# Optimization experiments

Measured on AMD Instinct MI355X. Metric: run time of the kernel, lower is better.

Reference implementation:

```python
import jax, jax.numpy as jnp
import numpy as np

B, S, E, H = 2, 2048, 1024, 16
DH = E // H  # 64
FF = 4 * E


def setup_inputs() -> dict:
    key = jax.random.key(0)
    ks = jax.random.split(key, 13)
    s = 0.02
    return {
        "x": jax.random.normal(ks[0], (B, S, E), dtype=jnp.float32),
        "Wq": jax.random.normal(ks[1], (H, E, DH), dtype=jnp.float32) * s,
        "Wk": jax.random.normal(ks[2], (H, E, DH), dtype=jnp.float32) * s,
        "Wv": jax.random.normal(ks[3], (H, E, DH), dtype=jnp.float32) * s,
        "Wo": jax.random.normal(ks[4], (E, E), dtype=jnp.float32) * s,
        "bo": jnp.zeros((E,), dtype=jnp.float32),
        "W1": jax.random.normal(ks[5], (E, FF), dtype=jnp.float32) * s,
        "b1": jnp.zeros((FF,), dtype=jnp.float32),
        "W2": jax.random.normal(ks[6], (FF, E), dtype=jnp.float32) * s,
        "b2": jnp.zeros((E,), dtype=jnp.float32),
        "g1": jnp.ones((E,), dtype=jnp.float32),
        "beta1": jnp.zeros((E,), dtype=jnp.float32),
        "g2": jnp.ones((E,), dtype=jnp.float32),
        "beta2": jnp.zeros((E,), dtype=jnp.float32),
    }


def _layernorm(x, g, b, eps=1e-5):
    mu = jnp.mean(x, axis=-1, keepdims=True)
    var = jnp.var(x, axis=-1, keepdims=True)
    return (x - mu) * jax.lax.rsqrt(var + eps) * g + b


def reference(x, Wq, Wk, Wv, Wo, bo, W1, b1, W2, b2, g1, beta1, g2, beta2):
    # Pre-LN attention (dropout is identity in eval mode)
    nx = _layernorm(x, g1, beta1)
    # per-head projections, batched over heads: [B,H,S,DH]
    q = jnp.einsum('bse,hed->bhsd', nx, Wq)
    k = jnp.einsum('bse,hed->bhsd', nx, Wk)
    v = jnp.einsum('bse,hed->bhsd', nx, Wv)
    scores = jnp.einsum('bhqd,bhkd->bhqk', q, k) * (DH ** -0.5)  # [B,H,S,S]
    seq = x.shape[1]
    causal = jnp.tril(jnp.ones((seq, seq), dtype=bool))
    scores = jnp.where(causal, scores, -jnp.inf)
    w = jax.nn.softmax(scores, axis=-1)
    attn = jnp.einsum('bhqk,bhkd->bhqd', w, v)  # [B,H,S,DH]
    # concat heads (head order matches ModuleList cat order)
    attn = attn.transpose(0, 2, 1, 3).reshape(x.shape[0], seq, E)
    attn_out = attn @ Wo + bo
    x = x + attn_out
    # FFN
    nx2 = _layernorm(x, g2, beta2)
    ffn = jax.nn.relu(nx2 @ W1 + b1) @ W2 + b2
    return x + ffn
```

## Files before the change

kernel.cpp:

```cpp
#include <hip/hip_runtime.h>


typedef __attribute__((ext_vector_type(8))) short short8;
typedef __attribute__((ext_vector_type(4))) float floatx4;

__device__ inline unsigned short f32_to_bf16(float f) {
  unsigned u = __float_as_uint(f);
  unsigned rb = (u >> 16) & 1u;
  u += 0x7fffu + rb;
  return (unsigned short)(u >> 16);
}
__device__ inline unsigned f32_to_bf16_hi(float f) {
  return (__float_as_uint(f) + 0x8000u) >> 16;
}
__device__ inline float bf16_to_f32(unsigned short u) {
  return __uint_as_float(((unsigned)u) << 16);
}

__device__ inline void gload16(const void* g, void* l) {
  __builtin_amdgcn_global_load_lds(
      (const __attribute__((address_space(1))) void*)g,
      (__attribute__((address_space(3))) void*)l, 16, 0, 0);
}

__global__ __launch_bounds__(256) void transpose_to_bf16(
    const float* __restrict__ in, unsigned short* __restrict__ out,
    int R, int C, int ldo, long in_bs, long out_bs) {
  __shared__ float tile[32][33];
  in  += (size_t)blockIdx.z * in_bs;
  out += (size_t)blockIdx.z * out_bs;
  const int c0 = blockIdx.x * 32, r0 = blockIdx.y * 32;
  const int tx = threadIdx.x & 31, ty = threadIdx.x >> 5;
#pragma unroll
  for (int i = 0; i < 32; i += 8)
    tile[ty + i][tx] = in[(size_t)(r0 + ty + i) * C + c0 + tx];
  __syncthreads();
#pragma unroll
  for (int i = 0; i < 32; i += 8)
    out[(size_t)(c0 + ty + i) * ldo + r0 + tx] = f32_to_bf16(tile[tx][ty + i]);
}

__global__ __launch_bounds__(256) void transpose_qkv_to_bf16(
    const float* __restrict__ Wq, const float* __restrict__ Wk,
    const float* __restrict__ Wv, unsigned short* __restrict__ out) {
  __shared__ float tile[32][33];
  const int z = blockIdx.z, m = z >> 4;
  const float* in = (m == 0 ? Wq : (m == 1 ? Wk : Wv)) + (size_t)(z & 15) * 65536;
  unsigned short* o = out + (size_t)z * 65536;
  const int c0 = blockIdx.x * 32, r0 = blockIdx.y * 32;
  const int tx = threadIdx.x & 31, ty = threadIdx.x >> 5;
#pragma unroll
  for (int i = 0; i < 32; i += 8)
    tile[ty + i][tx] = in[(size_t)(r0 + ty + i) * 64 + c0 + tx];
  __syncthreads();
#pragma unroll
  for (int i = 0; i < 32; i += 8)
    o[(size_t)(c0 + ty + i) * 1024 + r0 + tx] = f32_to_bf16(tile[tx][ty + i]);
}

__global__ __launch_bounds__(256) void transpose_v(
    const unsigned short* __restrict__ qkv, unsigned short* __restrict__ vT) {
  __shared__ unsigned short tile[32][33];
  const int bh = blockIdx.z, b = bh >> 4, h = bh & 15;
  const int k0 = blockIdx.x * 32, d0 = blockIdx.y * 32;
  const int tx = threadIdx.x & 31, ty = threadIdx.x >> 5;
#pragma unroll
  for (int i = 0; i < 32; i += 8)
    tile[ty + i][tx] = qkv[(size_t)(b * 2048 + k0 + ty + i) * 3072 + 2048 + h * 64 + d0 + tx];
  __syncthreads();
#pragma unroll
  for (int i = 0; i < 32; i += 8)
    vT[((size_t)bh * 64 + d0 + ty + i) * 2048 + k0 + tx] = tile[tx][ty + i];
}

__global__ __launch_bounds__(256) void layernorm_bf16(
    const float* __restrict__ x, const float* __restrict__ g,
    const float* __restrict__ be, unsigned short* __restrict__ out) {
  const int row = blockIdx.x;
  const int t = threadIdx.x;
  floatx4 v = ((const floatx4*)(x + (size_t)row * 1024))[t];
  float s  = v[0] + v[1] + v[2] + v[3];
  float s2 = v[0]*v[0] + v[1]*v[1] + v[2]*v[2] + v[3]*v[3];
#pragma unroll
  for (int off = 1; off < 64; off <<= 1) {
    s  += __shfl_xor(s, off);
    s2 += __shfl_xor(s2, off);
  }
  __shared__ float red[8];
  const int wave = t >> 6, lane = t & 63;
  if (lane == 0) { red[wave] = s; red[wave + 4] = s2; }
  __syncthreads();
  float ts  = red[0] + red[1] + red[2] + red[3];
  float ts2 = red[4] + red[5] + red[6] + red[7];
  float mu  = ts * (1.f / 1024.f);
  float var = ts2 * (1.f / 1024.f) - mu * mu;
  float rs  = rsqrtf(var + 1e-5f);
  floatx4 gv = ((const floatx4*)g)[t];
  floatx4 bv = ((const floatx4*)be)[t];
  ushort4 ov;
  ov.x = f32_to_bf16((v[0] - mu) * rs * gv[0] + bv[0]);
  ov.y = f32_to_bf16((v[1] - mu) * rs * gv[1] + bv[1]);
  ov.z = f32_to_bf16((v[2] - mu) * rs * gv[2] + bv[2]);
  ov.w = f32_to_bf16((v[3] - mu) * rs * gv[3] + bv[3]);
  ((ushort4*)(out + (size_t)row * 1024))[t] = ov;
}

#define STAGE_HALF(PTR, LDSARR, H, KTT)                                        \
  {                                                                            \
    gload16(PTR + (size_t)((H) * 128) * Kfull + (KTT) * 64,                    \
            &LDSARR[(H) * 8192 + ldsb]);                                       \
    gload16(PTR + (size_t)((H) * 128 + 8) * Kfull + (KTT) * 64,                \
            &LDSARR[(H) * 8192 + ldsb + 512]);                                 \
  }

#define PHASE_COMPUTE(Q)                                                       \
  {                                                                            \
    short8 af[2][2];                                                           \
    _Pragma("unroll") for (int ii = 0; ii < 2; ++ii)                           \
      _Pragma("unroll") for (int kk = 0; kk < 2; ++kk)                         \
        af[ii][kk] = *(const short8*)&As[s][(wm + ((Q) * 2 + ii) * 16 + l15) * 64 + \
                                            (((kk * 4 + quad) ^ rsw) * 8)];    \
    __builtin_amdgcn_s_setprio(1);                                             \
    _Pragma("unroll") for (int ii = 0; ii < 2; ++ii)                           \
      _Pragma("unroll") for (int j = 0; j < 4; ++j)                            \
        _Pragma("unroll") for (int kk = 0; kk < 2; ++kk)                       \
          acc[(Q) * 2 + ii][j] = __builtin_amdgcn_mfma_f32_16x16x32_bf16(      \
              af[ii][kk], bfr[j][kk], acc[(Q) * 2 + ii][j], 0, 0, 0);          \
    __builtin_amdgcn_s_setprio(0);                                             \
  }

__global__ __launch_bounds__(512, 2) void gemm256_bf16(
    const unsigned short* __restrict__ A, const unsigned short* __restrict__ Bt,
    const float* __restrict__ bias, unsigned short* __restrict__ Cout,
    int M, int N, int Kfull, int mode) {
  __shared__ unsigned short As[2][256 * 64];
  __shared__ unsigned short Bs[2][256 * 64];
  const int t = threadIdx.x;
  const int lane = t & 63, wave = t >> 6;
  const int l15 = lane & 15, quad = lane >> 4;
  const int wm = (wave >> 2) * 128, wn = (wave & 3) * 64;
  const int rsw = l15 & 7;

  const int cpx = gridDim.x >> 3;
  const int wgid = ((int)blockIdx.x & 7) * cpx + ((int)blockIdx.x >> 3);
  const int NBN = N >> 8;
  const int m0 = (wgid / NBN) << 8;
  const int n0 = (wgid % NBN) << 8;

  floatx4 acc[8][4];
#pragma unroll
  for (int i = 0; i < 8; ++i)
#pragma unroll
    for (int j = 0; j < 4; ++j) acc[i][j] = floatx4{0.f, 0.f, 0.f, 0.f};

  const int rr = lane >> 3, cc7 = lane & 7;
  const unsigned short* Ap = A + (size_t)(m0 + wave * 16 + rr) * Kfull + (cc7 ^ rr) * 8;
  const unsigned short* Bp = Bt + (size_t)(n0 + wave * 16 + rr) * Kfull + (cc7 ^ rr) * 8;
  const int ldsb = wave * 1024;

  const int KT = Kfull >> 6;
  STAGE_HALF(Ap, As[0], 0, 0)
  STAGE_HALF(Ap, As[0], 1, 0)
  STAGE_HALF(Bp, Bs[0], 0, 0)
  STAGE_HALF(Bp, Bs[0], 1, 0)

  for (int kt = 0; kt < KT; ++kt) {
    const int s = kt & 1, sx = s ^ 1;
    const bool st = (kt + 1 < KT);
    if (st) {
      STAGE_HALF(Ap, As[sx], 0, kt + 1)
      asm volatile("s_waitcnt vmcnt(2)" ::: "memory");
    } else {
      asm volatile("s_waitcnt vmcnt(0)" ::: "memory");
    }
    __builtin_amdgcn_s_barrier();
    short8 bfr[4][2];
#pragma unroll
    for (int j = 0; j < 4; ++j)
#pragma unroll
      for (int kk = 0; kk < 2; ++kk)
        bfr[j][kk] = *(const short8*)&Bs[s][(wn + j * 16 + l15) * 64 +
                                            (((kk * 4 + quad) ^ rsw) * 8)];
    PHASE_COMPUTE(0)
    if (st) STAGE_HALF(Ap, As[sx], 1, kt + 1)
    PHASE_COMPUTE(1)
    if (st) STAGE_HALF(Bp, Bs[sx], 0, kt + 1)
    PHASE_COMPUTE(2)
    if (st) STAGE_HALF(Bp, Bs[sx], 1, kt + 1)
    PHASE_COMPUTE(3)
    __builtin_amdgcn_s_barrier();
  }
  __builtin_amdgcn_sched_barrier(0);

  float bv[4] = {0.f, 0.f, 0.f, 0.f};
  if (mode) {
#pragma unroll
    for (int j = 0; j < 4; ++j) bv[j] = bias[n0 + wn + j * 16 + l15];
  }
  unsigned short* Cw = (wave < 4) ? (&As[0][0] + wave * 8192)
                                  : (&Bs[0][0] + (wave - 4) * 8192);
#pragma unroll
  for (int i = 0; i < 8; ++i)
#pragma unroll
    for (int j = 0; j < 4; ++j)
#pragma unroll
      for (int r = 0; r < 4; ++r) {
        float v = acc[i][j][r];
        if (mode) v = fmaxf(v + bv[j], 0.f);
        Cw[(i * 16 + quad * 4 + r) * 64 + j * 16 + l15] = f32_to_bf16(v);
      }
  unsigned short* Cg = Cout + (size_t)(m0 + wm) * N + n0 + wn;
#pragma unroll
  for (int c = 0; c < 16; ++c) {
    const int idx = c * 64 + lane;
    const int row = idx >> 3, c8 = idx & 7;
    *(uint4*)&Cg[(size_t)row * N + c8 * 8] = *(const uint4*)&Cw[row * 64 + c8 * 8];
  }
}

__global__ __launch_bounds__(256, 4) void gemm_bf16(
    const unsigned short* __restrict__ A, const unsigned short* __restrict__ Bt,
    const float* __restrict__ bias, const float* __restrict__ resid,
    void* __restrict__ Cout, int M, int N, int Kfull, int Klen, int mode) {
  __shared__ unsigned short As[2][128 * 32];
  __shared__ unsigned short Bs[2][128 * 32];
  const int t = threadIdx.x;
  const int NB = gridDim.x;
  const int bid = blockIdx.y * NB + blockIdx.x;
  const int xcd = bid & 7, slot = bid >> 3;
  const int m0 = (xcd * 4 + slot / NB) * 128;
  const int n0 = (slot % NB) * 128;
  const int koff = blockIdx.z * Klen;
  const int lane = t & 63, wave = t >> 6;
  const int wm = (wave >> 1) * 64, wn = (wave & 1) * 64;
  const int l15 = lane & 15, quad = lane >> 4;

  floatx4 acc[4][4];
#pragma unroll
  for (int i = 0; i < 4; ++i)
#pragma unroll
    for (int j = 0; j < 4; ++j) acc[i][j] = floatx4{0.f, 0.f, 0.f, 0.f};

  const int srow = wave * 32 + (lane >> 2);
  const int scol = (lane & 3) * 8;
  const unsigned short* Ag0 = A + (size_t)(m0 + srow) * Kfull + koff + scol;
  const unsigned short* Ag1 = Ag0 + (size_t)16 * Kfull;
  const unsigned short* Bg0 = Bt + (size_t)(n0 + srow) * Kfull + koff + scol;
  const unsigned short* Bg1 = Bg0 + (size_t)16 * Kfull;
  const int sbase0 = (wave * 2 + 0) * 512;
  const int sbase1 = (wave * 2 + 1) * 512;

  const int KT = Klen >> 5;
  gload16(Ag0, &As[0][sbase0]);
  gload16(Ag1, &As[0][sbase1]);
  gload16(Bg0, &Bs[0][sbase0]);
  gload16(Bg1, &Bs[0][sbase1]);

  int buf = 0;
  for (int kt = 0; kt < KT; ++kt) {
    if (kt + 1 < KT) {
      const int ko = (kt + 1) * 32;
      gload16(Ag0 + ko, &As[buf ^ 1][sbase0]);
      gload16(Ag1 + ko, &As[buf ^ 1][sbase1]);
      gload16(Bg0 + ko, &Bs[buf ^ 1][sbase0]);
      gload16(Bg1 + ko, &Bs[buf ^ 1][sbase1]);
      asm volatile("s_waitcnt vmcnt(4)" ::: "memory");
    } else {
      asm volatile("s_waitcnt vmcnt(0)" ::: "memory");
    }
    __builtin_amdgcn_s_barrier();
    short8 a[4], b[4];
#pragma unroll
    for (int i = 0; i < 4; ++i)
      a[i] = *(const short8*)&As[buf][(wm + i * 16 + l15) * 32 + quad * 8];
#pragma unroll
    for (int i = 0; i < 4; ++i)
      b[i] = *(const short8*)&Bs[buf][(wn + i * 16 + l15) * 32 + quad * 8];
#pragma unroll
    for (int i = 0; i < 4; ++i)
#pragma unroll
      for (int j = 0; j < 4; ++j)
        acc[i][j] = __builtin_amdgcn_mfma_f32_16x16x32_bf16(a[i], b[j], acc[i][j], 0, 0, 0);
    __builtin_amdgcn_s_barrier();
    buf ^= 1;
  }
  __builtin_amdgcn_sched_barrier(0);

  const size_t poff = (size_t)blockIdx.z * 4096 * 1024;
#pragma unroll
  for (int i = 0; i < 4; ++i)
#pragma unroll
    for (int j = 0; j < 4; ++j) {
      const int col = n0 + wn + j * 16 + l15;
      const int rb = m0 + wm + i * 16 + quad * 4;
#pragma unroll
      for (int r = 0; r < 4; ++r) {
        const int row = rb + r;
        float v = acc[i][j][r];
        if (mode == 1) {
          v += bias[col] + resid[(size_t)row * N + col];
          ((float*)Cout)[(size_t)row * N + col] = v;
        } else {
          ((float*)Cout)[poff + (size_t)row * N + col] = v;
        }
      }
    }
}

__global__ __launch_bounds__(256) void splitk_reduce(
    const float* __restrict__ p, const float* __restrict__ bias,
    const float* __restrict__ resid, float* __restrict__ out) {
  const int t = threadIdx.x;
  const size_t base = (size_t)blockIdx.x * 256 + t;
  floatx4 a = ((const floatx4*)p)[base];
  floatx4 b = ((const floatx4*)p)[1048576 + base];
  floatx4 rv = ((const floatx4*)resid)[base];
  floatx4 bv = ((const floatx4*)bias)[t];
  ((floatx4*)out)[base] = a + b + rv + bv;
}

__global__ __launch_bounds__(256) void splitk_reduce_ln(
    const float* __restrict__ p, const float* __restrict__ bias,
    const float* __restrict__ resid, const float* __restrict__ g,
    const float* __restrict__ be, float* __restrict__ xout,
    unsigned short* __restrict__ nxout) {
  const int row = blockIdx.x, t = threadIdx.x;
  const size_t base = (size_t)row * 256 + t;
  floatx4 a = ((const floatx4*)p)[base];
  floatx4 b = ((const floatx4*)p)[1048576 + base];
  floatx4 rv = ((const floatx4*)resid)[base];
  floatx4 bv = ((const floatx4*)bias)[t];
  floatx4 v = a + b + rv + bv;
  ((floatx4*)xout)[base] = v;
  float s  = v[0] + v[1] + v[2] + v[3];
  float s2 = v[0]*v[0] + v[1]*v[1] + v[2]*v[2] + v[3]*v[3];
#pragma unroll
  for (int off = 1; off < 64; off <<= 1) {
    s  += __shfl_xor(s, off);
    s2 += __shfl_xor(s2, off);
  }
  __shared__ float red[8];
  const int wave = t >> 6, lane = t & 63;
  if (lane == 0) { red[wave] = s; red[wave + 4] = s2; }
  __syncthreads();
  float ts  = red[0] + red[1] + red[2] + red[3];
  float ts2 = red[4] + red[5] + red[6] + red[7];
  float mu  = ts * (1.f / 1024.f);
  float var = ts2 * (1.f / 1024.f) - mu * mu;
  float rs  = rsqrtf(var + 1e-5f);
  floatx4 gv = ((const floatx4*)g)[t];
  floatx4 bev = ((const floatx4*)be)[t];
  ushort4 ov;
  ov.x = f32_to_bf16((v[0] - mu) * rs * gv[0] + bev[0]);
  ov.y = f32_to_bf16((v[1] - mu) * rs * gv[1] + bev[1]);
  ov.z = f32_to_bf16((v[2] - mu) * rs * gv[2] + bev[2]);
  ov.w = f32_to_bf16((v[3] - mu) * rs * gv[3] + bev[3]);
  ((ushort4*)(nxout + (size_t)row * 1024))[t] = ov;
}

__global__ __launch_bounds__(256, 3) void flash_attn_mfma(
    const unsigned short* __restrict__ qkv,
    const unsigned short* __restrict__ vT,
    unsigned short* __restrict__ attn) {
  const int id = blockIdx.x;
  const int xcd = id & 7, slot = id >> 3;
  const int bh = xcd * 4 + (slot & 3);
  const int qt = 15 - (slot >> 2);
  const int b = bh >> 4, h = bh & 15;
  const int q0 = qt * 128;
  const int t = threadIdx.x;
  const int wave = t >> 6, lane = t & 63;
  const int l15 = lane & 15, quad = lane >> 4;

  __shared__ unsigned short Ks[2][64][68];
  __shared__ unsigned short Vs[2][64][68];
  __shared__ unsigned short Ps[4][32][68];

  const size_t qbase = (size_t)b * 2048 * 3072;
  const int qrow_w = q0 + wave * 32;
  const unsigned short* Kbase = qkv + qbase + 1024 + h * 64;
  const unsigned short* Vbase = vT + (size_t)bh * 64 * 2048;

  short8 qf[2][2];
#pragma unroll
  for (int mf = 0; mf < 2; ++mf)
#pragma unroll
    for (int kc = 0; kc < 2; ++kc) {
      short8 raw = *(const short8*)(qkv + qbase +
          (size_t)(qrow_w + mf * 16 + l15) * 3072 + h * 64 + kc * 32 + quad * 8);
      short8 sc;
#pragma unroll
      for (int j = 0; j < 8; ++j)
        sc[j] = (short)f32_to_bf16(bf16_to_f32((unsigned short)raw[j]) * 0.125f);
      qf[mf][kc] = sc;
    }

  floatx4 o[2][4];
  float l_s[2] = {0.f, 0.f};
#pragma unroll
  for (int mf = 0; mf < 2; ++mf)
#pragma unroll
    for (int jd = 0; jd < 4; ++jd) o[mf][jd] = floatx4{0.f, 0.f, 0.f, 0.f};

  const int sr = t >> 3, so = (t & 7) * 8;

  uint4 kr0 = *(const uint4*)(Kbase + (size_t)sr * 3072 + so);
  uint4 kr1 = *(const uint4*)(Kbase + (size_t)(sr + 32) * 3072 + so);
  uint4 vr0 = *(const uint4*)(Vbase + (size_t)sr * 2048 + so);
  uint4 vr1 = *(const uint4*)(Vbase + (size_t)(sr + 32) * 2048 + so);

  const int ntiles = 2 * qt + 2;
  int buf = 0;
  for (int kt = 0; kt < ntiles; ++kt) {
    const int k0 = kt * 64;
    *(uint4*)&Ks[buf][sr][so]      = kr0;
    *(uint4*)&Ks[buf][sr + 32][so] = kr1;
    *(uint4*)&Vs[buf][sr][so]      = vr0;
    *(uint4*)&Vs[buf][sr + 32][so] = vr1;
    if (kt + 1 < ntiles) {
      const int k1 = k0 + 64;
      kr0 = *(const uint4*)(Kbase + (size_t)(k1 + sr) * 3072 + so);
      kr1 = *(const uint4*)(Kbase + (size_t)(k1 + sr + 32) * 3072 + so);
      vr0 = *(const uint4*)(Vbase + (size_t)sr * 2048 + k1 + so);
      vr1 = *(const uint4*)(Vbase + (size_t)(sr + 32) * 2048 + k1 + so);
    }
    asm volatile("s_waitcnt lgkmcnt(0)" ::: "memory");
    __builtin_amdgcn_s_barrier();

    if (k0 <= qrow_w + 31) {
      short8 kf[2][4];
#pragma unroll
      for (int kc = 0; kc < 2; ++kc)
#pragma unroll
        for (int jb = 0; jb < 4; ++jb)
          kf[kc][jb] = *(const short8*)&Ks[buf][jb * 16 + l15][kc * 32 + quad * 8];

      floatx4 st[2][4];
#pragma unroll
      for (int mf = 0; mf < 2; ++mf)
#pragma unroll
        for (int jb = 0; jb < 4; ++jb) st[mf][jb] = floatx4{0.f, 0.f, 0.f, 0.f};
      __builtin_amdgcn_s_setprio(1);
#pragma unroll
      for (int kc = 0; kc < 2; ++kc)
#pragma unroll
        for (int jb = 0; jb < 4; ++jb) {
#pragma unroll
          for (int mf = 0; mf < 2; ++mf)
            st[mf][jb] = __builtin_amdgcn_mfma_f32_16x16x32_bf16(
                kf[kc][jb], qf[mf][kc], st[mf][jb], 0, 0, 0);
        }
      __builtin_amdgcn_s_setprio(0);

#pragma unroll
      for (int mf = 0; mf < 2; ++mf) {
        const int qq = qrow_w + mf * 16 + l15;
#pragma unroll
        for (int jb = 0; jb < 4; ++jb) {
          const int keyb = k0 + jb * 16 + quad * 4;
          float p0 = (keyb + 0 > qq) ? 0.f : __expf(st[mf][jb][0]);
          float p1 = (keyb + 1 > qq) ? 0.f : __expf(st[mf][jb][1]);
          float p2 = (keyb + 2 > qq) ? 0.f : __expf(st[mf][jb][2]);
          float p3 = (keyb + 3 > qq) ? 0.f : __expf(st[mf][jb][3]);
          l_s[mf] += (p0 + p1) + (p2 + p3);
          uint2 pk;
          pk.x = (f32_to_bf16_hi(p1) << 16) | f32_to_bf16_hi(p0);
          pk.y = (f32_to_bf16_hi(p3) << 16) | f32_to_bf16_hi(p2);
          *(uint2*)&Ps[wave][mf * 16 + l15][jb * 16 + quad * 4] = pk;
        }
      }

      __builtin_amdgcn_s_setprio(1);
#pragma unroll
      for (int kc = 0; kc < 2; ++kc) {
        short8 pf0 = *(const short8*)&Ps[wave][l15][kc * 32 + quad * 8];
        short8 pf1 = *(const short8*)&Ps[wave][16 + l15][kc * 32 + quad * 8];
#pragma unroll
        for (int jd = 0; jd < 4; ++jd) {
          short8 vf = *(const short8*)&Vs[buf][jd * 16 + l15][kc * 32 + quad * 8];
          o[0][jd] = __builtin_amdgcn_mfma_f32_16x16x32_bf16(pf0, vf, o[0][jd], 0, 0, 0);
          o[1][jd] = __builtin_amdgcn_mfma_f32_16x16x32_bf16(pf1, vf, o[1][jd], 0, 0, 0);
        }
      }
      __builtin_amdgcn_s_setprio(0);
    }
    buf ^= 1;
  }

#pragma unroll
  for (int mf = 0; mf < 2; ++mf) {
    l_s[mf] += __shfl_xor(l_s[mf], 16);
    l_s[mf] += __shfl_xor(l_s[mf], 32);
  }

#pragma unroll
  for (int mf = 0; mf < 2; ++mf)
#pragma unroll
    for (int r = 0; r < 4; ++r) {
      const int qloc = quad * 4 + r;
      const float lsum = __shfl(l_s[mf], qloc);
      const float rl = 1.f / lsum;
      const int row = b * 2048 + q0 + wave * 32 + mf * 16 + qloc;
#pragma unroll
      for (int jd = 0; jd < 4; ++jd)
        attn[(size_t)row * 1024 + h * 64 + jd * 16 + l15] =
            f32_to_bf16(o[mf][jd][r] * rl);
    }
}

extern "C" void kernel_launch(void* const* d_in, const int* in_sizes, int n_in,
                              void* d_out, int out_size, void* d_ws, size_t ws_size,
                              hipStream_t stream) {
  const float* x   = (const float*)d_in[0];
  const float* Wq  = (const float*)d_in[1];
  const float* Wk  = (const float*)d_in[2];
  const float* Wv  = (const float*)d_in[3];
  const float* Wo  = (const float*)d_in[4];
  const float* bo  = (const float*)d_in[5];
  const float* W1  = (const float*)d_in[6];
  const float* b1  = (const float*)d_in[7];
  const float* W2  = (const float*)d_in[8];
  const float* b2  = (const float*)d_in[9];
  const float* g1  = (const float*)d_in[10];
  const float* be1 = (const float*)d_in[11];
  const float* g2  = (const float*)d_in[12];
  const float* be2 = (const float*)d_in[13];
  float* out = (float*)d_out;

  char* ws = (char*)d_ws;
  size_t off = 0;
  auto alloc = [&](size_t bytes) -> void* {
    void* p = ws + off;
    off += (bytes + 255) & ~(size_t)255;
    return p;
  };
  unsigned short* WqkvT = (unsigned short*)alloc(3072ull * 1024 * 2);
  unsigned short* WoT   = (unsigned short*)alloc(1024ull * 1024 * 2);
  unsigned short* W1T   = (unsigned short*)alloc(4096ull * 1024 * 2);
  unsigned short* W2T   = (unsigned short*)alloc(1024ull * 4096 * 2);
  unsigned short* nx    = (unsigned short*)alloc(4096ull * 1024 * 2);
  unsigned short* qkv   = (unsigned short*)alloc(4096ull * 3072 * 2);
  unsigned short* attn  = (unsigned short*)alloc(4096ull * 1024 * 2);
  float*          x1    = (float*)alloc(4096ull * 1024 * 4);
  unsigned short* nx2   = (unsigned short*)alloc(4096ull * 1024 * 2);
  unsigned short* hbuf  = (unsigned short*)alloc(4096ull * 4096 * 2);
  unsigned short* vT    = hbuf;
  float*          part  = (float*)nx;

  dim3 blk(256);
  transpose_qkv_to_bf16<<<dim3(2, 32, 48), blk, 0, stream>>>(Wq, Wk, Wv, WqkvT);
  transpose_to_bf16<<<dim3(32, 32, 1), blk, 0, stream>>>(Wo, WoT, 1024, 1024, 1024, 0, 0);
  transpose_to_bf16<<<dim3(128, 32, 1), blk, 0, stream>>>(W1, W1T, 1024, 4096, 1024, 0, 0);
  transpose_to_bf16<<<dim3(32, 128, 1), blk, 0, stream>>>(W2, W2T, 4096, 1024, 4096, 0, 0);

  layernorm_bf16<<<4096, blk, 0, stream>>>(x, g1, be1, nx);
  gemm256_bf16<<<dim3(192), dim3(512), 0, stream>>>(nx, WqkvT, nullptr, qkv, 4096, 3072, 1024, 0);
  transpose_v<<<dim3(64, 2, 32), blk, 0, stream>>>(qkv, vT);
  flash_attn_mfma<<<dim3(512, 1, 1), blk, 0, stream>>>(qkv, vT, attn);
  gemm_bf16<<<dim3(8, 32, 2), blk, 0, stream>>>(attn, WoT, nullptr, nullptr, part, 4096, 1024, 1024, 512, 3);
  splitk_reduce_ln<<<4096, blk, 0, stream>>>(part, bo, x, g2, be2, x1, nx2);
  gemm256_bf16<<<dim3(256), dim3(512), 0, stream>>>(nx2, W1T, b1, hbuf, 4096, 4096, 1024, 1);
  gemm_bf16<<<dim3(8, 32, 2), blk, 0, stream>>>(hbuf, W2T, nullptr, nullptr, part, 4096, 1024, 4096, 2048, 3);
  splitk_reduce<<<4096, blk, 0, stream>>>(part, b2, x1, out);
}
```

Measured before the change: 362.5 us.

## Use split-K 4 with bf16 partials staged through LDS for coalesced stores

The Wo and W2 GEMMs now split K four ways instead of two. Their partial sums are written as bf16 rather than fp32, and the epilogue first stages each tile in LDS and then writes it to global memory as coalesced 16-byte rows. The reduce kernels read and sum four bf16 partials. The aim is more parallelism (more blocks) and less partial-sum traffic with better store coalescing, at the cost of precision loss from rounding the partial sums to bf16.

```diff
diff --git a/kernel.cpp b/kernel.cpp
--- a/kernel.cpp
+++ b/kernel.cpp
@@ -286,52 +286,100 @@
   }
   __builtin_amdgcn_sched_barrier(0);
 
-  const size_t poff = (size_t)blockIdx.z * 4096 * 1024;
-#pragma unroll
-  for (int i = 0; i < 4; ++i)
-#pragma unroll
-    for (int j = 0; j < 4; ++j) {
-      const int col = n0 + wn + j * 16 + l15;
-      const int rb = m0 + wm + i * 16 + quad * 4;
-#pragma unroll
-      for (int r = 0; r < 4; ++r) {
-        const int row = rb + r;
-        float v = acc[i][j][r];
-        if (mode == 1) {
-          v += bias[col] + resid[(size_t)row * N + col];
-          ((float*)Cout)[(size_t)row * N + col] = v;
-        } else {
-          ((float*)Cout)[poff + (size_t)row * N + col] = v;
+  if (mode == 0 || mode == 2 || mode == 4) {
+    unsigned short* Cb = (unsigned short*)Cout +
+                         (mode == 4 ? (size_t)blockIdx.z * 4096 * 1024 : 0);
+    unsigned short* Cs = &As[0][0];
+#pragma unroll
+    for (int p = 0; p < 2; ++p) {
+      if ((wm >> 6) == p) {
+#pragma unroll
+        for (int i = 0; i < 4; ++i)
+#pragma unroll
+          for (int j = 0; j < 4; ++j)
+#pragma unroll
+            for (int r = 0; r < 4; ++r) {
+              const int rl = i * 16 + quad * 4 + r;
+              float v = acc[i][j][r];
+              if (mode == 2) {
+                v += bias[n0 + wn + j * 16 + l15];
+                v = fmaxf(v, 0.f);
+              }
+              Cs[rl * 128 + wn + j * 16 + l15] = f32_to_bf16(v);
+            }
+      }
+      __syncthreads();
+#pragma unroll
+      for (int c = 0; c < 4; ++c) {
+        const int idx = c * 256 + t;
+        const int row = idx >> 4, chunk = idx & 15;
+        *(uint4*)&Cb[(size_t)(m0 + p * 64 + row) * N + n0 + chunk * 8] =
+            *(const uint4*)&Cs[row * 128 + chunk * 8];
+      }
+      __syncthreads();
+    }
+  } else {
+    const size_t poff = (size_t)blockIdx.z * 4096 * 1024;
+#pragma unroll
+    for (int i = 0; i < 4; ++i)
+#pragma unroll
+      for (int j = 0; j < 4; ++j) {
+        const int col = n0 + wn + j * 16 + l15;
+        const int rb = m0 + wm + i * 16 + quad * 4;
+#pragma unroll
+        for (int r = 0; r < 4; ++r) {
+          const int row = rb + r;
+          float v = acc[i][j][r];
+          if (mode == 1) {
+            v += bias[col] + resid[(size_t)row * N + col];
+            ((float*)Cout)[(size_t)row * N + col] = v;
+          } else {
+            ((float*)Cout)[poff + (size_t)row * N + col] = v;
+          }
         }
       }
-    }
-}
-
-__global__ __launch_bounds__(256) void splitk_reduce(
-    const float* __restrict__ p, const float* __restrict__ bias,
+  }
+}
+
+__global__ __launch_bounds__(256) void splitk4_reduce(
+    const unsigned short* __restrict__ p, const float* __restrict__ bias,
     const float* __restrict__ resid, float* __restrict__ out) {
-  const int t = threadIdx.x;
-  const size_t base = (size_t)blockIdx.x * 256 + t;
-  floatx4 a = ((const floatx4*)p)[base];
-  floatx4 b = ((const floatx4*)p)[1048576 + base];
-  floatx4 rv = ((const floatx4*)resid)[base];
+  const int t = threadIdx.x, row = blockIdx.x;
+  const size_t base = (size_t)row * 1024 + t * 4;
+  ushort4 a0 = *(const ushort4*)&p[base];
+  ushort4 a1 = *(const ushort4*)&p[4194304 + base];
+  ushort4 a2 = *(const ushort4*)&p[2 * 4194304 + base];
+  ushort4 a3 = *(const ushort4*)&p[3 * 4194304 + base];
+  floatx4 rv = ((const floatx4*)resid)[base >> 2];
   floatx4 bv = ((const floatx4*)bias)[t];
-  ((floatx4*)out)[base] = a + b + rv + bv;
-}
-
-__global__ __launch_bounds__(256) void splitk_reduce_ln(
-    const float* __restrict__ p, const float* __restrict__ bias,
+  floatx4 v;
+  v[0] = bf16_to_f32(a0.x) + bf16_to_f32(a1.x) + bf16_to_f32(a2.x) + bf16_to_f32(a3.x);
+  v[1] = bf16_to_f32(a0.y) + bf16_to_f32(a1.y) + bf16_to_f32(a2.y) + bf16_to_f32(a3.y);
+  v[2] = bf16_to_f32(a0.z) + bf16_to_f32(a1.z) + bf16_to_f32(a2.z) + bf16_to_f32(a3.z);
+  v[3] = bf16_to_f32(a0.w) + bf16_to_f32(a1.w) + bf16_to_f32(a2.w) + bf16_to_f32(a3.w);
+  ((floatx4*)out)[base >> 2] = v + rv + bv;
+}
+
+__global__ __launch_bounds__(256) void splitk4_reduce_ln(
+    const unsigned short* __restrict__ p, const float* __restrict__ bias,
     const float* __restrict__ resid, const float* __restrict__ g,
     const float* __restrict__ be, float* __restrict__ xout,
     unsigned short* __restrict__ nxout) {
   const int row = blockIdx.x, t = threadIdx.x;
-  const size_t base = (size_t)row * 256 + t;
-  floatx4 a = ((const floatx4*)p)[base];
-  floatx4 b = ((const floatx4*)p)[1048576 + base];
-  floatx4 rv = ((const floatx4*)resid)[base];
+  const size_t base = (size_t)row * 1024 + t * 4;
+  ushort4 a0 = *(const ushort4*)&p[base];
+  ushort4 a1 = *(const ushort4*)&p[4194304 + base];
+  ushort4 a2 = *(const ushort4*)&p[2 * 4194304 + base];
+  ushort4 a3 = *(const ushort4*)&p[3 * 4194304 + base];
+  floatx4 rv = ((const floatx4*)resid)[base >> 2];
   floatx4 bv = ((const floatx4*)bias)[t];
-  floatx4 v = a + b + rv + bv;
-  ((floatx4*)xout)[base] = v;
+  floatx4 v;
+  v[0] = bf16_to_f32(a0.x) + bf16_to_f32(a1.x) + bf16_to_f32(a2.x) + bf16_to_f32(a3.x);
+  v[1] = bf16_to_f32(a0.y) + bf16_to_f32(a1.y) + bf16_to_f32(a2.y) + bf16_to_f32(a3.y);
+  v[2] = bf16_to_f32(a0.z) + bf16_to_f32(a1.z) + bf16_to_f32(a2.z) + bf16_to_f32(a3.z);
+  v[3] = bf16_to_f32(a0.w) + bf16_to_f32(a1.w) + bf16_to_f32(a2.w) + bf16_to_f32(a3.w);
+  v = v + rv + bv;
+  ((floatx4*)xout)[base >> 2] = v;
   float s  = v[0] + v[1] + v[2] + v[3];
   float s2 = v[0]*v[0] + v[1]*v[1] + v[2]*v[2] + v[3]*v[3];
 #pragma unroll
@@ -545,7 +593,7 @@
   unsigned short* nx2   = (unsigned short*)alloc(4096ull * 1024 * 2);
   unsigned short* hbuf  = (unsigned short*)alloc(4096ull * 4096 * 2);
   unsigned short* vT    = hbuf;
-  float*          part  = (float*)nx;
+  unsigned short* partbf = (unsigned short*)nx;
 
   dim3 blk(256);
   transpose_qkv_to_bf16<<<dim3(2, 32, 48), blk, 0, stream>>>(Wq, Wk, Wv, WqkvT);
@@ -557,9 +605,9 @@
   gemm256_bf16<<<dim3(192), dim3(512), 0, stream>>>(nx, WqkvT, nullptr, qkv, 4096, 3072, 1024, 0);
   transpose_v<<<dim3(64, 2, 32), blk, 0, stream>>>(qkv, vT);
   flash_attn_mfma<<<dim3(512, 1, 1), blk, 0, stream>>>(qkv, vT, attn);
-  gemm_bf16<<<dim3(8, 32, 2), blk, 0, stream>>>(attn, WoT, nullptr, nullptr, part, 4096, 1024, 1024, 512, 3);
-  splitk_reduce_ln<<<4096, blk, 0, stream>>>(part, bo, x, g2, be2, x1, nx2);
+  gemm_bf16<<<dim3(8, 32, 4), blk, 0, stream>>>(attn, WoT, nullptr, nullptr, partbf, 4096, 1024, 1024, 256, 4);
+  splitk4_reduce_ln<<<4096, blk, 0, stream>>>(partbf, bo, x, g2, be2, x1, nx2);
   gemm256_bf16<<<dim3(256), dim3(512), 0, stream>>>(nx2, W1T, b1, hbuf, 4096, 4096, 1024, 1);
-  gemm_bf16<<<dim3(8, 32, 2), blk, 0, stream>>>(hbuf, W2T, nullptr, nullptr, part, 4096, 1024, 4096, 2048, 3);
-  splitk_reduce<<<4096, blk, 0, stream>>>(part, b2, x1, out);
-}
+  gemm_bf16<<<dim3(8, 32, 4), blk, 0, stream>>>(hbuf, W2T, nullptr, nullptr, partbf, 4096, 1024, 4096, 1024, 4);
+  splitk4_reduce<<<4096, blk, 0, stream>>>(partbf, b2, x1, out);
+}
```

Measured after the change: 370.0 us. 2.1% more time.
